# Optimization experiments

Measured on AMD Instinct MI355X. Metric: run time of the kernel, lower is better.

Reference implementation:

```python
import jax, jax.numpy as jnp
import numpy as np

B, T, C = 4, 2048, 1024
NQ, D = 8, C // 8  # n_query heads, head dim = n_embd // 8


def setup_inputs() -> dict:
    key = jax.random.key(0)
    ks = jax.random.split(key, 6)
    s = 0.02
    return {
        "x": jax.random.normal(ks[0], (B, T, C), dtype=jnp.float32),
        "Wk": jax.random.normal(ks[1], (C, D), dtype=jnp.float32) * s,
        "Wv": jax.random.normal(ks[2], (C, D), dtype=jnp.float32) * s,
        "Wq": jax.random.normal(ks[3], (NQ, C, D), dtype=jnp.float32) * s,
        "Wp": jax.random.normal(ks[4], (NQ * D, C), dtype=jnp.float32) * s,
        "bp": jnp.zeros((C,), dtype=jnp.float32),
    }


def reference(x, Wk, Wv, Wq, Wp, bp):
    b, t, c = x.shape
    scale = c ** -0.5  # original scales by n_embd**-0.5, not head-dim
    k = x @ Wk                                   # [B,T,D] shared across heads (MQA)
    v = x @ Wv                                   # [B,T,D]
    q = jnp.einsum("btc,qcd->bqtd", x, Wq)       # [B,NQ,T,D]
    wei = jnp.einsum("bqtd,bsd->bqts", q, k) * scale
    causal = jnp.tril(jnp.ones((t, t), dtype=bool))
    wei = jnp.where(causal, wei, -jnp.inf)
    wei = jax.nn.softmax(wei, axis=-1)
    out = jnp.einsum("bqts,bsd->btqd", wei, v)   # [B,T,NQ,D]
    out = out.reshape(b, t, -1)                  # concat heads -> [B,T,NQ*D]
    return out @ Wp + bp
```

## Files before the change

### kernel.cpp

```cpp
#include <hip/hip_runtime.h>
#include <hip/hip_bf16.h>
#include <cstddef>
#include <cstdint>

#define B 4
#define T 2048
#define C 1024
#define NQ 8
#define D 128
#define M_ROWS (B * T)
#define NTOT (2 * D + NQ * D)

typedef __bf16 bf16x8 __attribute__((ext_vector_type(8)));
typedef float  f32x4  __attribute__((ext_vector_type(4)));
typedef uint32_t u32x4 __attribute__((ext_vector_type(4)));

__device__ __forceinline__ ushort f2bf(float f) {
    union { float f; uint32_t u; } v; v.f = f;
    const uint32_t r = (v.u + 0x7fffu + ((v.u >> 16) & 1u)) >> 16;
    return (ushort)r;
}

__device__ __forceinline__ uint32_t cvt_pk_bf16(float lo, float hi) {
    uint32_t r;
    asm("v_cvt_pk_bf16_f32 %0, %1, %2" : "=v"(r) : "v"(lo), "v"(hi));
    return r;
}

__device__ __forceinline__ void gld_lds16(const ushort* g, ushort* lds_uniform) {
    __builtin_amdgcn_global_load_lds(
        (const __attribute__((address_space(1))) void*)g,
        (__attribute__((address_space(3))) void*)lds_uniform, 16, 0, 0);
}

__global__ __launch_bounds__(256) void xcvt(const float* __restrict__ x,
                                            ushort* __restrict__ xb) {
    const size_t i = ((size_t)blockIdx.x * 256 + threadIdx.x) * 8;
    const float4 a = *(const float4*)(x + i);
    const float4 b = *(const float4*)(x + i + 4);
    uint4 o;
    o.x = f2bf(a.x) | ((uint32_t)f2bf(a.y) << 16);
    o.y = f2bf(a.z) | ((uint32_t)f2bf(a.w) << 16);
    o.z = f2bf(b.x) | ((uint32_t)f2bf(b.y) << 16);
    o.w = f2bf(b.z) | ((uint32_t)f2bf(b.w) << 16);
    *(uint4*)(xb + i) = o;
}

__device__ __forceinline__ void wtrans_body(const float* __restrict__ src,
                                            ushort* __restrict__ dst, int NC,
                                            int bx, int by) {
    __shared__ ushort Ts[64][72];
    const int tid = threadIdx.x;
    const int k0 = by * 64, c0 = bx * 64;
    {
        const int r = tid >> 2, cq = tid & 3;
#pragma unroll
        for (int i = 0; i < 4; ++i) {
            const int cc = cq * 16 + i * 4;
            const float4 v = *(const float4*)(src + (size_t)(k0 + r) * NC + c0 + cc);
            uint2 o;
            o.x = f2bf(v.x) | ((uint32_t)f2bf(v.y) << 16);
            o.y = f2bf(v.z) | ((uint32_t)f2bf(v.w) << 16);
            *(uint2*)(&Ts[r][cc]) = o;
        }
    }
    __syncthreads();
    {
        const int n = tid >> 2, kq = tid & 3;
        ushort vv[16];
#pragma unroll
        for (int j = 0; j < 16; ++j) vv[j] = Ts[kq * 16 + j][n];
        uint4 o0, o1;
        o0.x = vv[0] | ((uint32_t)vv[1] << 16);  o0.y = vv[2] | ((uint32_t)vv[3] << 16);
        o0.z = vv[4] | ((uint32_t)vv[5] << 16);  o0.w = vv[6] | ((uint32_t)vv[7] << 16);
        o1.x = vv[8] | ((uint32_t)vv[9] << 16);  o1.y = vv[10] | ((uint32_t)vv[11] << 16);
        o1.z = vv[12] | ((uint32_t)vv[13] << 16); o1.w = vv[14] | ((uint32_t)vv[15] << 16);
        ushort* d = dst + (size_t)(c0 + n) * C + k0 + kq * 16;
        *(uint4*)d = o0;
        *(uint4*)(d + 8) = o1;
    }
}

__global__ __launch_bounds__(256) void wtrans_qkv(const float* __restrict__ Wk,
                                                  const float* __restrict__ Wv,
                                                  const float* __restrict__ Wq,
                                                  ushort* __restrict__ WcatT) {
    const int z = blockIdx.z;
    const float* src;
    int rbase;
    if (z == 0)      { src = Wk; rbase = 0; }
    else if (z == 1) { src = Wv; rbase = D; }
    else             { src = Wq + (size_t)(z - 2) * C * D; rbase = 2 * D + (z - 2) * D; }
    wtrans_body(src, WcatT + (size_t)rbase * C, D, blockIdx.x, blockIdx.y);
}

__global__ __launch_bounds__(256) void wtrans_p(const float* __restrict__ Wp,
                                                ushort* __restrict__ WpT) {
    wtrans_body(Wp, WpT, C, blockIdx.x, blockIdx.y);
}

__global__ __launch_bounds__(256) void vtrans(const ushort* __restrict__ qkv,
                                              ushort* __restrict__ vbT) {
    __shared__ ushort Ts[64][136];
    const int tid = threadIdx.x;
    const int kb0 = blockIdx.x * 64;
    {
        const int r = tid >> 2, cq = tid & 3;
        const ushort* src = qkv + (size_t)(kb0 + r) * NTOT + D;
#pragma unroll
        for (int i = 0; i < 4; ++i) {
            const int cc = (cq * 4 + i) * 8;
            *(uint4*)(&Ts[r][cc]) = *(const uint4*)(src + cc);
        }
    }
    __syncthreads();
    {
        const int d = tid >> 1, half = tid & 1;
        ushort vv[32];
#pragma unroll
        for (int k = 0; k < 32; ++k) vv[k] = Ts[half * 32 + k][d];
        uint32_t dw[16];
#pragma unroll
        for (int i = 0; i < 16; ++i) {
            const int p0 = 2 * i, p1 = 2 * i + 1;
            const int k0 = (p0 & 3) | (((p0 >> 3) & 3) << 2) | (((p0 >> 2) & 1) << 4);
            const int k1 = (p1 & 3) | (((p1 >> 3) & 3) << 2) | (((p1 >> 2) & 1) << 4);
            dw[i] = vv[k0] | ((uint32_t)vv[k1] << 16);
        }
        uint32_t* dst = (uint32_t*)(vbT + (size_t)d * M_ROWS + kb0 + half * 32);
#pragma unroll
        for (int i = 0; i < 4; ++i)
            *(uint4*)(dst + i * 4) = *(uint4*)(&dw[i * 4]);
    }
}

template <bool BF16_OUT>
__global__ __launch_bounds__(256) void gemm_mfma(const ushort* __restrict__ A,
                                                 const ushort* __restrict__ Bt,
                                                 void* __restrict__ Cout,
                                                 const float* __restrict__ bias,
                                                 const int Nout) {
    __shared__ ushort As[128 * 32];
    __shared__ ushort Bs[128 * 32];
    const int tid  = threadIdx.x;
    const int lane = tid & 63;
    const int w    = tid >> 6;
    const int col  = lane & 15;
    const int quad = lane >> 4;
    const int row0 = blockIdx.y * 128;
    const int col0 = blockIdx.x * 128;
    const int wm = w & 1, wn = w >> 1;

    const int srow = lane >> 2;
    const int skk  = (lane & 3) * 8;

    f32x4 acc[4][4];
#pragma unroll
    for (int i = 0; i < 4; ++i)
#pragma unroll
        for (int j = 0; j < 4; ++j) acc[i][j] = (f32x4){0.f, 0.f, 0.f, 0.f};

    for (int k0 = 0; k0 < C; k0 += 32) {
        __syncthreads();
#pragma unroll
        for (int j = 0; j < 2; ++j) {
            const int ci = w * 2 + j;
            const int r  = ci * 16 + srow;
            gld_lds16(A  + (size_t)(row0 + r) * C + k0 + skk, &As[ci * 512]);
            gld_lds16(Bt + (size_t)(col0 + r) * C + k0 + skk, &Bs[ci * 512]);
        }
        __syncthreads();

        bf16x8 af[4], bfr[4];
#pragma unroll
        for (int i = 0; i < 4; ++i)
            af[i] = *(const bf16x8*)&As[(wm * 64 + i * 16 + col) * 32 + quad * 8];
#pragma unroll
        for (int j = 0; j < 4; ++j)
            bfr[j] = *(const bf16x8*)&Bs[(wn * 64 + j * 16 + col) * 32 + quad * 8];
#pragma unroll
        for (int i = 0; i < 4; ++i)
#pragma unroll
            for (int j = 0; j < 4; ++j)
                acc[i][j] = __builtin_amdgcn_mfma_f32_16x16x32_bf16(af[i], bfr[j], acc[i][j], 0, 0, 0);
    }

#pragma unroll
    for (int i = 0; i < 4; ++i) {
#pragma unroll
        for (int r = 0; r < 4; ++r) {
            const int grow = row0 + wm * 64 + i * 16 + quad * 4 + r;
#pragma unroll
            for (int j = 0; j < 4; ++j) {
                const int gcol = col0 + wn * 64 + j * 16 + col;
                const float v = acc[i][j][r];
                if (BF16_OUT) {
                    ((ushort*)Cout)[(size_t)grow * Nout + gcol] = f2bf(v);
                } else {
                    ((float*)Cout)[(size_t)grow * Nout + gcol] = v + bias[gcol];
                }
            }
        }
    }
}

__global__ __launch_bounds__(512, 2) void attn_mfma(const ushort* __restrict__ qkv,
                                                    const ushort* __restrict__ vbT,
                                                    ushort* __restrict__ attb) {
    __shared__ ushort SMEM[32768];

    const int tid  = threadIdx.x;
    const int lane = tid & 63;
    const int w    = tid >> 6;
    const int g    = w >> 2;
    const int w2   = w & 3;
    const int col  = lane & 15;
    const int quad = lane >> 4;
    const int h    = blockIdx.y;
    const int b    = blockIdx.z;
    const int p    = blockIdx.x;
    const int sShort = p, sLong = 15 - p;
    const int own_nt = 4 * p + 4;

    const ushort* kraw = qkv + (size_t)b * T * NTOT;
    const ushort* vraw = vbT + (size_t)b * T;

    bf16x8 qf[2][4];
    auto loadQ = [&](int strip) {
#pragma unroll
        for (int qs = 0; qs < 2; ++qs) {
            const ushort* qrow = qkv + (size_t)(b * T + strip * 128 + w2 * 32 + qs * 16 + col) * NTOT
                                 + 2 * D + h * D;
#pragma unroll
            for (int kb2 = 0; kb2 < 4; ++kb2)
                qf[qs][kb2] = *(const bf16x8*)(qrow + kb2 * 32 + quad * 8);
        }
    };
    loadQ(g == 0 ? sShort : sLong);

    f32x4 O[2][8];
    float l_acc[2];
    auto resetAcc = [&]() {
#pragma unroll
        for (int qs = 0; qs < 2; ++qs) {
            l_acc[qs] = 0.f;
#pragma unroll
            for (int i = 0; i < 8; ++i) O[qs][i] = (f32x4){0.f, 0.f, 0.f, 0.f};
        }
    };
    resetAcc();

    const int sk_key = lane >> 2, sk_d = (lane & 3) * 8;
    const int sv_dr  = lane >> 1, sv_po = (lane & 1) * 8;
    const int kg0 = quad >> 1, ko = (quad & 1) * 8;
    const float SC = 0.045084220f;

    auto stage = [&](int bf, int kt) {
        ushort* Kd = SMEM + g * 16384 + bf * 4096 + w2 * 1024;
        ushort* Vd = SMEM + g * 16384 + 8192 + bf * 4096 + (w2 >> 1) * 2048 + (w2 & 1) * 1024;
#pragma unroll
        for (int half = 0; half < 2; ++half)
            gld_lds16(kraw + (size_t)(kt * 32 + half * 16 + sk_key) * NTOT + w2 * 32 + sk_d,
                      Kd + half * 512);
#pragma unroll
        for (int i2 = 0; i2 < 2; ++i2)
            gld_lds16(vraw + (size_t)((w2 & 1) * 64 + i2 * 32 + sv_dr) * M_ROWS
                           + kt * 32 + (w2 >> 1) * 16 + sv_po,
                      Vd + i2 * 512);
    };

    auto storeOut = [&](int qbase) {
#pragma unroll
        for (int qs = 0; qs < 2; ++qs) {
            float s = l_acc[qs];
            s += __shfl_xor(s, 16);
            s += __shfl_xor(s, 32);
#pragma unroll
            for (int r = 0; r < 4; ++r) {
                const float inv = 1.0f / __shfl(s, quad * 4 + r);
                const int t = qbase + w2 * 32 + qs * 16 + quad * 4 + r;
                ushort* orow = attb + (size_t)(b * T + t) * C + h * D;
#pragma unroll
                for (int nt = 0; nt < 8; ++nt)
                    orow[nt * 16 + col] = f2bf(O[qs][nt][r] * inv);
            }
        }
    };

    auto compute = [&](int bf, int kt, int qg) {
        const ushort* Kc = SMEM + g * 16384 + bf * 4096;
        const ushort* Vc = SMEM + g * 16384 + 8192 + bf * 4096;
        f32x4 S[2][2];
#pragma unroll
        for (int qs = 0; qs < 2; ++qs)
#pragma unroll
            for (int sub = 0; sub < 2; ++sub) S[qs][sub] = (f32x4){0.f, 0.f, 0.f, 0.f};
#pragma unroll
        for (int sub = 0; sub < 2; ++sub) {
#pragma unroll
            for (int kb2 = 0; kb2 < 4; ++kb2) {
                bf16x8 kf = *(const bf16x8*)(Kc + kb2 * 1024 + (sub * 16 + col) * 32 + quad * 8);
                S[0][sub] = __builtin_amdgcn_mfma_f32_16x16x32_bf16(kf, qf[0][kb2], S[0][sub], 0, 0, 0);
                S[1][sub] = __builtin_amdgcn_mfma_f32_16x16x32_bf16(kf, qf[1][kb2], S[1][sub], 0, 0, 0);
            }
        }

        const bool msk = (kt * 32 + 31 > qg);
        bf16x8 paf[2];
#pragma unroll
        for (int qs = 0; qs < 2; ++qs) {
            float pr[2][4];
            if (msk) {
                const int q = qg + w2 * 32 + qs * 16 + col;
#pragma unroll
                for (int sub = 0; sub < 2; ++sub)
#pragma unroll
                    for (int r = 0; r < 4; ++r) {
                        const int key = kt * 32 + sub * 16 + quad * 4 + r;
                        const float sc = (key > q) ? -1e30f : S[qs][sub][r] * SC;
                        pr[sub][r] = __builtin_amdgcn_exp2f(sc);
                    }
            } else {
#pragma unroll
                for (int sub = 0; sub < 2; ++sub)
#pragma unroll
                    for (int r = 0; r < 4; ++r)
                        pr[sub][r] = __builtin_amdgcn_exp2f(S[qs][sub][r] * SC);
            }
            l_acc[qs] += (pr[0][0] + pr[0][1]) + (pr[0][2] + pr[0][3])
                       + (pr[1][0] + pr[1][1]) + (pr[1][2] + pr[1][3]);
            u32x4 wpk;
            wpk.x = cvt_pk_bf16(pr[0][0], pr[0][1]);
            wpk.y = cvt_pk_bf16(pr[0][2], pr[0][3]);
            wpk.z = cvt_pk_bf16(pr[1][0], pr[1][1]);
            wpk.w = cvt_pk_bf16(pr[1][2], pr[1][3]);
            paf[qs] = __builtin_bit_cast(bf16x8, wpk);
        }

#pragma unroll
        for (int nt = 0; nt < 8; ++nt) {
            bf16x8 vf = *(const bf16x8*)(Vc + kg0 * 2048 + (nt * 16 + col) * 16 + ko);
            O[0][nt] = __builtin_amdgcn_mfma_f32_16x16x32_bf16(paf[0], vf, O[0][nt], 0, 0, 0);
            O[1][nt] = __builtin_amdgcn_mfma_f32_16x16x32_bf16(paf[1], vf, O[1][nt], 0, 0, 0);
        }
    };

    auto ktOf = [&](int j) {
        return (g == 1) ? j : (j < own_nt ? j : 34 + (j - own_nt));
    };

    int qg = (g == 0 ? sShort : sLong) * 128;

    stage(0, ktOf(0));
    __syncthreads();

    int cur = 0;
    for (int j = 0; j < 34; ++j) {
        if (j + 1 < 34) stage(cur ^ 1, ktOf(j + 1));
        if (g == 0 && j == own_nt) {
            storeOut(sShort * 128);
            resetAcc();
            loadQ(sLong);
            qg = sLong * 128;
        }
        compute(cur, ktOf(j), qg);
        __syncthreads();
        cur ^= 1;
    }

    float* Sf = (float*)SMEM;
    float ltot[2] = {0.f, 0.f};
    if (g == 0) {
#pragma unroll
        for (int qs = 0; qs < 2; ++qs) {
            float s = l_acc[qs];
            s += __shfl_xor(s, 16);
            s += __shfl_xor(s, 32);
            if (quad == 0) Sf[w2 * 32 + qs * 16 + col] = s;
        }
    }
    __syncthreads();
    if (g == 1) {
#pragma unroll
        for (int qs = 0; qs < 2; ++qs) {
            float s = l_acc[qs];
            s += __shfl_xor(s, 16);
            s += __shfl_xor(s, 32);
            ltot[qs] = s + Sf[w2 * 32 + qs * 16 + col];
        }
    }
    __syncthreads();
    if (g == 0) {
#pragma unroll
        for (int qs = 0; qs < 2; ++qs)
#pragma unroll
            for (int nt = 0; nt < 8; ++nt)
#pragma unroll
                for (int r = 0; r < 4; ++r)
                    Sf[(size_t)(w2 * 32 + qs * 16 + quad * 4 + r) * 128 + nt * 16 + col] = O[qs][nt][r];
    }
    __syncthreads();
    if (g == 1) {
#pragma unroll
        for (int qs = 0; qs < 2; ++qs) {
#pragma unroll
            for (int r = 0; r < 4; ++r) {
                const float inv = 1.0f / __shfl(ltot[qs], quad * 4 + r);
                const int qi = w2 * 32 + qs * 16 + quad * 4 + r;
                const int t = sLong * 128 + qi;
                ushort* orow = attb + (size_t)(b * T + t) * C + h * D;
#pragma unroll
                for (int nt = 0; nt < 8; ++nt)
                    orow[nt * 16 + col] =
                        f2bf((O[qs][nt][r] + Sf[(size_t)qi * 128 + nt * 16 + col]) * inv);
            }
        }
    }
}

extern "C" void kernel_launch(void* const* d_in, const int* in_sizes, int n_in,
                              void* d_out, int out_size, void* d_ws, size_t ws_size,
                              hipStream_t stream) {
    const float* x  = (const float*)d_in[0];
    const float* Wk = (const float*)d_in[1];
    const float* Wv = (const float*)d_in[2];
    const float* Wq = (const float*)d_in[3];
    const float* Wp = (const float*)d_in[4];
    const float* bp = (const float*)d_in[5];
    float* out = (float*)d_out;

    char* ws = (char*)d_ws;
    ushort* xb    = (ushort*)ws;
    ushort* attb  = xb;
    ushort* qkv   = (ushort*)(ws + (size_t)16  * 1024 * 1024);
    ushort* WcatT = (ushort*)(ws + (size_t)36  * 1024 * 1024);
    ushort* WpT   = (ushort*)(ws + (size_t)39  * 1024 * 1024);
    ushort* vbT   = (ushort*)(ws + (size_t)41  * 1024 * 1024);

    xcvt<<<(size_t)M_ROWS * C / (256 * 8), 256, 0, stream>>>(x, xb);
    wtrans_qkv<<<dim3(D / 64, C / 64, 2 + NQ), 256, 0, stream>>>(Wk, Wv, Wq, WcatT);
    wtrans_p<<<dim3(C / 64, C / 64), 256, 0, stream>>>(Wp, WpT);

    gemm_mfma<true><<<dim3(NTOT / 128, M_ROWS / 128), 256, 0, stream>>>(
        xb, WcatT, qkv, nullptr, NTOT);

    vtrans<<<M_ROWS / 64, 256, 0, stream>>>(qkv, vbT);

    attn_mfma<<<dim3(8, NQ, B), 512, 0, stream>>>(qkv, vbT, attb);

    gemm_mfma<false><<<dim3(C / 128, M_ROWS / 128), 256, 0, stream>>>(
        attb, WpT, out, bp, C);
}
```

Before: 220.8 us.

## Halve attention query strip to 64 rows, doubling grid with 256-thread blocks

The attention kernel now processes 64-row query strips per group instead of 128, using 4 waves per block (2 groups of 2) and launching 16×8×4 blocks instead of 8×8×4. Each wave stages twice as many K/V chunks, and the paired short/long strip split is rescaled to 33 iterations. The aim is more blocks for better load balance and occupancy across CUs. The cost is that K/V tiles are loaded once per 64 queries rather than per 128, doubling K/V traffic, while shared memory per block stays 64KB.

Result: no change. 218.5 us (-1.0%).

```diff
diff --git a/kernel.cpp b/kernel.cpp
--- a/kernel.cpp
+++ b/kernel.cpp
@@ -204,7 +204,7 @@
     }
 }
 
-__global__ __launch_bounds__(512, 2) void attn_mfma(const ushort* __restrict__ qkv,
+__global__ __launch_bounds__(256, 2) void attn_mfma(const ushort* __restrict__ qkv,
                                                     const ushort* __restrict__ vbT,
                                                     ushort* __restrict__ attb) {
     __shared__ ushort SMEM[32768];
@@ -212,15 +212,15 @@
     const int tid  = threadIdx.x;
     const int lane = tid & 63;
     const int w    = tid >> 6;
-    const int g    = w >> 2;
-    const int w2   = w & 3;
+    const int g    = w >> 1;
+    const int wq   = w & 1;
     const int col  = lane & 15;
     const int quad = lane >> 4;
     const int h    = blockIdx.y;
     const int b    = blockIdx.z;
-    const int p    = blockIdx.x;
-    const int sShort = p, sLong = 15 - p;
-    const int own_nt = 4 * p + 4;
+    const int x    = blockIdx.x;
+    const int sShort = x, sLong = 31 - x;
+    const int own_nt = 2 * x + 2;
 
     const ushort* kraw = qkv + (size_t)b * T * NTOT;
     const ushort* vraw = vbT + (size_t)b * T;
@@ -229,7 +229,7 @@
     auto loadQ = [&](int strip) {
 #pragma unroll
         for (int qs = 0; qs < 2; ++qs) {
-            const ushort* qrow = qkv + (size_t)(b * T + strip * 128 + w2 * 32 + qs * 16 + col) * NTOT
+            const ushort* qrow = qkv + (size_t)(b * T + strip * 64 + wq * 32 + qs * 16 + col) * NTOT
                                  + 2 * D + h * D;
 #pragma unroll
             for (int kb2 = 0; kb2 < 4; ++kb2)
@@ -255,21 +255,26 @@
     const int kg0 = quad >> 1, ko = (quad & 1) * 8;
     const float SC = 0.045084220f;
 
+    ushort* gbase = SMEM + g * 16384;
+
     auto stage = [&](int bf, int kt) {
-        ushort* Kd = SMEM + g * 16384 + bf * 4096 + w2 * 1024;
-        ushort* Vd = SMEM + g * 16384 + 8192 + bf * 4096 + (w2 >> 1) * 2048 + (w2 & 1) * 1024;
-#pragma unroll
-        for (int half = 0; half < 2; ++half)
-            gld_lds16(kraw + (size_t)(kt * 32 + half * 16 + sk_key) * NTOT + w2 * 32 + sk_d,
-                      Kd + half * 512);
-#pragma unroll
-        for (int i2 = 0; i2 < 2; ++i2)
-            gld_lds16(vraw + (size_t)((w2 & 1) * 64 + i2 * 32 + sv_dr) * M_ROWS
-                           + kt * 32 + (w2 >> 1) * 16 + sv_po,
-                      Vd + i2 * 512);
-    };
-
-    auto storeOut = [&](int qbase) {
+        ushort* Kd = gbase + bf * 4096;
+        ushort* Vd = gbase + 8192 + bf * 4096;
+#pragma unroll
+        for (int cc = 0; cc < 2; ++cc) {
+            const int c = wq * 2 + cc;
+#pragma unroll
+            for (int half = 0; half < 2; ++half)
+                gld_lds16(kraw + (size_t)(kt * 32 + half * 16 + sk_key) * NTOT + c * 32 + sk_d,
+                          Kd + c * 1024 + half * 512);
+        }
+#pragma unroll
+        for (int i2 = 0; i2 < 4; ++i2)
+            gld_lds16(vraw + (size_t)(i2 * 32 + sv_dr) * M_ROWS + kt * 32 + wq * 16 + sv_po,
+                      Vd + wq * 2048 + i2 * 512);
+    };
+
+    auto storeOut = [&](int strip) {
 #pragma unroll
         for (int qs = 0; qs < 2; ++qs) {
             float s = l_acc[qs];
@@ -278,7 +283,7 @@
 #pragma unroll
             for (int r = 0; r < 4; ++r) {
                 const float inv = 1.0f / __shfl(s, quad * 4 + r);
-                const int t = qbase + w2 * 32 + qs * 16 + quad * 4 + r;
+                const int t = strip * 64 + wq * 32 + qs * 16 + quad * 4 + r;
                 ushort* orow = attb + (size_t)(b * T + t) * C + h * D;
 #pragma unroll
                 for (int nt = 0; nt < 8; ++nt)
@@ -288,8 +293,8 @@
     };
 
     auto compute = [&](int bf, int kt, int qg) {
-        const ushort* Kc = SMEM + g * 16384 + bf * 4096;
-        const ushort* Vc = SMEM + g * 16384 + 8192 + bf * 4096;
+        const ushort* Kc = gbase + bf * 4096;
+        const ushort* Vc = gbase + 8192 + bf * 4096;
         f32x4 S[2][2];
 #pragma unroll
         for (int qs = 0; qs < 2; ++qs)
@@ -311,7 +316,7 @@
         for (int qs = 0; qs < 2; ++qs) {
             float pr[2][4];
             if (msk) {
-                const int q = qg + w2 * 32 + qs * 16 + col;
+                const int q = qg + wq * 32 + qs * 16 + col;
 #pragma unroll
                 for (int sub = 0; sub < 2; ++sub)
 #pragma unroll
@@ -346,29 +351,30 @@
     };
 
     auto ktOf = [&](int j) {
-        return (g == 1) ? j : (j < own_nt ? j : 34 + (j - own_nt));
-    };
-
-    int qg = (g == 0 ? sShort : sLong) * 128;
+        return (g == 1) ? j : (j < own_nt ? j : 33 + (j - own_nt));
+    };
+
+    int qg = (g == 0 ? sShort : sLong) * 64;
 
     stage(0, ktOf(0));
     __syncthreads();
 
     int cur = 0;
-    for (int j = 0; j < 34; ++j) {
-        if (j + 1 < 34) stage(cur ^ 1, ktOf(j + 1));
+    for (int j = 0; j < 33; ++j) {
+        if (j + 1 < 33) stage(cur ^ 1, ktOf(j + 1));
         if (g == 0 && j == own_nt) {
-            storeOut(sShort * 128);
+            storeOut(sShort);
             resetAcc();
             loadQ(sLong);
-            qg = sLong * 128;
+            qg = sLong * 64;
         }
         compute(cur, ktOf(j), qg);
         __syncthreads();
         cur ^= 1;
     }
 
-    float* Sf = (float*)SMEM;
+    float* Lf = (float*)SMEM;
+    float* Of = Lf + 64;
     float ltot[2] = {0.f, 0.f};
     if (g == 0) {
 #pragma unroll
@@ -376,7 +382,7 @@
             float s = l_acc[qs];
             s += __shfl_xor(s, 16);
             s += __shfl_xor(s, 32);
-            if (quad == 0) Sf[w2 * 32 + qs * 16 + col] = s;
+            if (quad == 0) Lf[wq * 32 + qs * 16 + col] = s;
         }
     }
     __syncthreads();
@@ -386,7 +392,7 @@
             float s = l_acc[qs];
             s += __shfl_xor(s, 16);
             s += __shfl_xor(s, 32);
-            ltot[qs] = s + Sf[w2 * 32 + qs * 16 + col];
+            ltot[qs] = s + Lf[wq * 32 + qs * 16 + col];
         }
     }
     __syncthreads();
@@ -397,7 +403,7 @@
             for (int nt = 0; nt < 8; ++nt)
 #pragma unroll
                 for (int r = 0; r < 4; ++r)
-                    Sf[(size_t)(w2 * 32 + qs * 16 + quad * 4 + r) * 128 + nt * 16 + col] = O[qs][nt][r];
+                    Of[(size_t)(wq * 32 + qs * 16 + quad * 4 + r) * 128 + nt * 16 + col] = O[qs][nt][r];
     }
     __syncthreads();
     if (g == 1) {
@@ -406,13 +412,13 @@
 #pragma unroll
             for (int r = 0; r < 4; ++r) {
                 const float inv = 1.0f / __shfl(ltot[qs], quad * 4 + r);
-                const int qi = w2 * 32 + qs * 16 + quad * 4 + r;
-                const int t = sLong * 128 + qi;
+                const int qi = wq * 32 + qs * 16 + quad * 4 + r;
+                const int t = sLong * 64 + qi;
                 ushort* orow = attb + (size_t)(b * T + t) * C + h * D;
 #pragma unroll
                 for (int nt = 0; nt < 8; ++nt)
                     orow[nt * 16 + col] =
-                        f2bf((O[qs][nt][r] + Sf[(size_t)qi * 128 + nt * 16 + col]) * inv);
+                        f2bf((O[qs][nt][r] + Of[(size_t)qi * 128 + nt * 16 + col]) * inv);
             }
         }
     }
@@ -446,7 +452,7 @@
 
     vtrans<<<M_ROWS / 64, 256, 0, stream>>>(qkv, vbT);
 
-    attn_mfma<<<dim3(8, NQ, B), 512, 0, stream>>>(qkv, vbT, attb);
+    attn_mfma<<<dim3(16, NQ, B), 256, 0, stream>>>(qkv, vbT, attb);
 
     gemm_mfma<false><<<dim3(C / 128, M_ROWS / 128), 256, 0, stream>>>(
         attb, WpT, out, bp, C);
```
